# Optimization experiments

Hardware: AMD Instinct MI355X
Metric: run time of the kernel (lower is better)

Reference implementation:

```python
import jax, jax.numpy as jnp
import numpy as np

B, N, H = 32, 256, 1024
HEADS, NHID = 8, 128
NCLS = 7
BAND = 24
ALPHA = 0.2          # GAT leaky-relu slope
NEG = -9e15          # masked-attention fill, as in pyGAT


def setup_inputs() -> dict:
    key = jax.random.key(0)
    ks = jax.random.split(key, 16)
    def nrm(k, shp, s=0.02):
        return jax.random.normal(k, shp, dtype=jnp.float32) * s
    hidden_cls = jax.random.normal(ks[0], (B, N, H), dtype=jnp.float32)
    hidden_emo = jax.random.normal(ks[1], (B, N, H), dtype=jnp.float32)
    # causal band cliques, diagonal included (GAT uses clique - eye)
    t = jnp.arange(N)
    band = ((t[None, :] <= t[:, None]) & (t[None, :] > t[:, None] - BAND)).astype(jnp.float32)
    clique = jnp.broadcast_to(band, (B, N, N))
    labels = jax.random.randint(ks[2], (B, N), 0, NCLS)
    pooler_W = nrm(ks[3], (H, H)); pooler_b = jnp.zeros((H,), jnp.float32)
    gat_W = nrm(ks[4], (HEADS, H, NHID))
    gat_a1 = nrm(ks[5], (HEADS, NHID)); gat_a2 = nrm(ks[6], (HEADS, NHID))
    out_W = nrm(ks[7], (H, H))            # heads*nhid == H -> nclass=H
    out_a1 = nrm(ks[8], (H,)); out_a2 = nrm(ks[9], (H,))
    lin1_W = nrm(ks[10], (H, H)); lin1_b = jnp.zeros((H,), jnp.float32)
    lin0_W = nrm(ks[11], (2 * H, H)); lin0_b = jnp.zeros((H,), jnp.float32)
    cls_W = nrm(ks[12], (H, NCLS)); cls_b = jnp.zeros((NCLS,), jnp.float32)
    A = jax.random.uniform(ks[13], (NCLS, NCLS), dtype=jnp.float32) + 0.1
    hmm_A = A / A.sum(axis=1, keepdims=True)   # row-stochastic transition matrix
    return dict(hidden_cls=hidden_cls, hidden_emo=hidden_emo, clique=clique,
                labels=labels, pooler_W=pooler_W, pooler_b=pooler_b,
                gat_W=gat_W, gat_a1=gat_a1, gat_a2=gat_a2,
                out_W=out_W, out_a1=out_a1, out_a2=out_a2,
                lin1_W=lin1_W, lin1_b=lin1_b, lin0_W=lin0_W, lin0_b=lin0_b,
                cls_W=cls_W, cls_b=cls_b, hmm_A=hmm_A)


def _lrelu(x):
    return jnp.where(x > 0, x, ALPHA * x)


def reference(hidden_cls, hidden_emo, clique, labels, pooler_W, pooler_b,
              gat_W, gat_a1, gat_a2, out_W, out_a1, out_a2,
              lin1_W, lin1_b, lin0_W, lin0_b, cls_W, cls_b, hmm_A):
    # PoolerAll: dense + tanh on all token states (dropout = identity in eval)
    fea_cls = jnp.tanh(hidden_cls @ pooler_W + pooler_b)   # [B,N,H] (CLS per utt)
    fea_emo = jnp.tanh(hidden_emo @ pooler_W + pooler_b)   # [B,N,H] (mask tok per utt)

    eyeN = jnp.eye(N, dtype=clique.dtype)
    adjm = (clique - eyeN) > 0                             # [B,N,N] GAT adjacency

    def gat_one(x, am):                                    # x [N,H], am [N,N]
        Wh = jnp.einsum('nf,hfd->hnd', x, gat_W)           # [heads,N,nhid]
        e = _lrelu(jnp.einsum('hnd,hd->hn', Wh, gat_a1)[:, :, None]
                   + jnp.einsum('hnd,hd->hn', Wh, gat_a2)[:, None, :])
        att = jax.nn.softmax(jnp.where(am[None], e, NEG), axis=-1)
        h1 = jax.nn.elu(jnp.einsum('hnm,hmd->hnd', att, Wh))
        h1 = jnp.transpose(h1, (1, 0, 2)).reshape(N, HEADS * NHID)
        Wh2 = h1 @ out_W                                   # out attention layer (concat=False)
        e2 = _lrelu((Wh2 @ out_a1)[:, None] + (Wh2 @ out_a2)[None, :])
        h2 = jax.nn.softmax(jnp.where(am, e2, NEG), axis=-1) @ Wh2
        return jax.nn.elu(h2)                              # [N,H]

    gat_out = jax.vmap(gat_one)(fea_cls, adjm)             # [B,N,H]
    # row 0 replaced by (dropout of) fea_cls row 0, as in the original
    g = jnp.concatenate([fea_cls[:, :1], gat_out[:, 1:]], axis=1)
    g = jnp.concatenate([fea_cls, g @ lin1_W + lin1_b], axis=-1) @ lin0_W + lin0_b
    log_gat = jax.nn.softmax(g @ cls_W + cls_b, axis=-1)   # [B,N,NCLS] (probs)

    # HMM emission probs hmm_B(fea) = softmax(classifier(fea))
    Bprob = jax.nn.softmax(fea_emo @ cls_W + cls_b, axis=-1)  # [B,N,NCLS]
    P0 = jnp.full((NCLS,), 1.0 / NCLS, dtype=jnp.float32)
    AT = hmm_A.T

    def hmm_row(Bp, mrow):                                 # Bp [N,NCLS], mrow [N]
        def step(carry, xs):
            p, started = carry
            bt, m = xs
            p_init = P0 * bt; p_init = p_init / p_init.sum()
            p_tr = (AT @ p) * bt; p_tr = p_tr / p_tr.sum()
            p_new = jnp.where(started, p_tr, p_init)
            valid = m > 0.5
            return (jnp.where(valid, p_new, p), started | valid), None
        (p, _), _ = jax.lax.scan(step, (P0, jnp.asarray(False)), (Bp, mrow))
        return p                                           # final filtered posterior

    log_hmm = jax.vmap(lambda Bp, M: jax.vmap(lambda mr: hmm_row(Bp, mr))(M))(Bprob, clique)

    logits = jnp.log((log_gat + log_hmm) * 0.5).reshape(B * N, NCLS)
    lab = labels.reshape(B * N)
    mask = lab >= 0
    picked = jnp.take_along_axis(logits, jnp.where(mask, lab, 0)[:, None], axis=1)[:, 0]
    loss = -(jnp.where(mask, picked, 0.0).sum() / jnp.maximum(mask.sum(), 1).astype(jnp.float32))
    return loss, logits
```

## Files before the change

### kernel.cpp

```cpp
#include <hip/hip_runtime.h>
#include <hip/hip_bf16.h>
#include <math.h>

typedef __hip_bfloat16 bf16;
typedef __attribute__((ext_vector_type(8))) short short8;
typedef __attribute__((ext_vector_type(4))) float float4v;

static constexpr int Bb = 32, Nn = 256, Hh = 1024, HEADS = 8, NHID = 128, NCLS = 7, BAND = 24;
static constexpr int M = Bb * Nn;
static constexpr float ALPHA = 0.2f;
static constexpr long INEL = (long)M * Hh;

__device__ __forceinline__ float tof(bf16 x) { return __bfloat162float(x); }
__device__ __forceinline__ bf16 tob(float x) { return __float2bfloat16(x); }
__device__ __forceinline__ unsigned short f2bits(float x) {
    bf16 h = __float2bfloat16(x);
    return *(unsigned short*)&h;
}
__device__ __forceinline__ float bits2f(unsigned short u) {
    unsigned v = ((unsigned)u) << 16;
    float f;
    __builtin_memcpy(&f, &v, 4);
    return f;
}

__device__ __forceinline__ void gload16(const void* g, void* l) {
    __builtin_amdgcn_global_load_lds(
        (const __attribute__((address_space(1))) void*)g,
        (__attribute__((address_space(3))) void*)l, 16, 0, 0);
}

static constexpr long OFF_PWT  = 0;
static constexpr long OFF_PB   = 1048576;
static constexpr long OFF_WCT  = 1049600;
static constexpr long OFF_GA1  = 2098176;
static constexpr long OFF_GA2  = 2099200;
static constexpr long OFF_OWT  = 2100224;
static constexpr long OFF_OA1  = 3148800;
static constexpr long OFF_OA2  = 3149824;
static constexpr long OFF_L1WT = 3150848;
static constexpr long OFF_L1B  = 4199424;
static constexpr long OFF_L0WT = 4200448;
static constexpr long OFF_L0B  = 6297600;
static constexpr long OFF_CWT  = 6298624;
static constexpr long OFF_CB   = 6305792;
static constexpr long OFF_HA   = 6305799;
static constexpr long W_TOTAL  = 6305848;

__global__ void probe_k(const void* __restrict__ p, int* __restrict__ flag) {
    int t = threadIdx.x;
    int bad = 0;
    for (int i = t; i < 4096; i += 256) {
        float v = tof(((const bf16*)p)[i]);
        if (!(fabsf(v) < 1e4f)) bad = 1;
    }
    __shared__ int sb[256];
    sb[t] = bad; __syncthreads();
    for (int s = 128; s; s >>= 1) { if (t < s) sb[t] |= sb[t + s]; __syncthreads(); }
    if (t == 0) *flag = sb[0] ? 0 : 1;
}

__device__ __forceinline__ float ldany(const void* p, long i, int isb) {
    return isb ? tof(((const bf16*)p)[i]) : ((const float*)p)[i];
}

__global__ void convert_k(const int* __restrict__ flagp,
                          const void* pW, const void* pb, const void* gW,
                          const void* ga1, const void* ga2, const void* oW,
                          const void* oa1, const void* oa2, const void* l1W,
                          const void* l1b, const void* l0W, const void* l0b,
                          const void* cW, const void* cb, const void* hA,
                          bf16* __restrict__ dst) {
    long idx = (long)blockIdx.x * 256 + threadIdx.x;
    if (idx >= W_TOTAL) return;
    int isb = *flagp;
    const void* src; long si;
    if      (idx < OFF_PB)   { long l = idx;            long n = l >> 10, k = l & 1023;
                               src = pW;  si = k * 1024 + n; }
    else if (idx < OFF_WCT)  { src = pb;  si = idx - OFF_PB; }
    else if (idx < OFF_GA1)  { long l = idx - OFF_WCT;  long n = l >> 10, f = l & 1023;
                               long h = n >> 7, d = n & 127;
                               src = gW;  si = h * 131072 + f * 128 + d; }
    else if (idx < OFF_GA2)  { src = ga1; si = idx - OFF_GA1; }
    else if (idx < OFF_OWT)  { src = ga2; si = idx - OFF_GA2; }
    else if (idx < OFF_OA1)  { long l = idx - OFF_OWT;  long n = l >> 10, k = l & 1023;
                               src = oW;  si = k * 1024 + n; }
    else if (idx < OFF_OA2)  { src = oa1; si = idx - OFF_OA1; }
    else if (idx < OFF_L1WT) { src = oa2; si = idx - OFF_OA2; }
    else if (idx < OFF_L1B)  { long l = idx - OFF_L1WT; long n = l >> 10, k = l & 1023;
                               src = l1W; si = k * 1024 + n; }
    else if (idx < OFF_L0WT) { src = l1b; si = idx - OFF_L1B; }
    else if (idx < OFF_L0B)  { long l = idx - OFF_L0WT; long n = l >> 11, k = l & 2047;
                               src = l0W; si = k * 1024 + n; }
    else if (idx < OFF_CWT)  { src = l0b; si = idx - OFF_L0B; }
    else if (idx < OFF_CB)   { long l = idx - OFF_CWT;  long c = l >> 10, k = l & 1023;
                               src = cW;  si = k * 7 + c; }
    else if (idx < OFF_HA)   { src = cb;  si = idx - OFF_CB; }
    else                     { src = hA;  si = idx - OFF_HA; }
    dst[idx] = tob(ldany(src, si, isb));
}

__global__ void convin_k(const int* __restrict__ flagp, const void* __restrict__ s0,
                         const void* __restrict__ s1, bf16* __restrict__ d0,
                         bf16* __restrict__ d1) {
    const int isb = *flagp;
    long i = ((long)blockIdx.x * 256 + threadIdx.x) * 8;
    const void* s; bf16* d; long off;
    if (i < INEL) { s = s0; d = d0; off = i; }
    else          { s = s1; d = d1; off = i - INEL; }
    if (isb) {
        *(int4*)(d + off) = *(const int4*)((const bf16*)s + off);
    } else {
        const float* f = (const float*)s + off;
        unsigned short tmp[8];
        #pragma unroll
        for (int q = 0; q < 8; ++q) tmp[q] = f2bits(f[q]);
        *(int4*)(d + off) = *(int4*)tmp;
    }
}

template <int ACT>
__device__ __forceinline__ void gemm_core(const bf16* __restrict__ A,
                                          const bf16* __restrict__ Bt,
                                          const bf16* __restrict__ bias,
                                          bf16* __restrict__ Cout,
                                          unsigned short* As, unsigned short* Bs,
                                          int Nc, int K, int bm, int bn) {
    const int tid = threadIdx.x;
    const int lane = tid & 63;
    const int wave = tid >> 6;
    const int wm = (wave >> 1) * 64, wn = (wave & 1) * 64;
    const int l15 = lane & 15, quad = lane >> 4;
    const int r0 = wave * 32;
    const int lrow = lane >> 2, q = lane & 3;
    const int rA = r0 + lrow, rB = r0 + 16 + lrow;
    const int qa = (q ^ (rA & 3) ^ ((rA >> 2) & 3)) * 8;
    const int qb = (q ^ (rB & 3) ^ ((rB >> 2) & 3)) * 8;
    const int sc8 = (quad ^ (l15 & 3) ^ (l15 >> 2)) * 8;

    float4v acc[4][4];
    #pragma unroll
    for (int i = 0; i < 4; ++i)
        #pragma unroll
        for (int j = 0; j < 4; ++j) acc[i][j] = (float4v){0.f, 0.f, 0.f, 0.f};

    const bf16* ga0 = A + (long)(bm + rA) * K + qa;
    const bf16* ga1 = A + (long)(bm + rB) * K + qb;
    const bf16* gb0 = Bt + (long)(bn + rA) * K + qa;
    const bf16* gb1 = Bt + (long)(bn + rB) * K + qb;

    for (int k0 = 0; k0 < K; k0 += 64) {
        gload16(ga0 + k0,      As + r0 * 32);
        gload16(ga1 + k0,      As + (r0 + 16) * 32);
        gload16(ga0 + k0 + 32, As + 4096 + r0 * 32);
        gload16(ga1 + k0 + 32, As + 4096 + (r0 + 16) * 32);
        gload16(gb0 + k0,      Bs + r0 * 32);
        gload16(gb1 + k0,      Bs + (r0 + 16) * 32);
        gload16(gb0 + k0 + 32, Bs + 4096 + r0 * 32);
        gload16(gb1 + k0 + 32, Bs + 4096 + (r0 + 16) * 32);
        __syncthreads();
        #pragma unroll
        for (int ks = 0; ks < 2; ++ks) {
            const unsigned short* Au = As + ks * 4096;
            const unsigned short* Bu = Bs + ks * 4096;
            short8 af[4], bfr[4];
            #pragma unroll
            for (int i = 0; i < 4; ++i)
                af[i] = *(const short8*)(Au + (wm + i * 16 + l15) * 32 + sc8);
            #pragma unroll
            for (int j = 0; j < 4; ++j)
                bfr[j] = *(const short8*)(Bu + (wn + j * 16 + l15) * 32 + sc8);
            #pragma unroll
            for (int i = 0; i < 4; ++i)
                #pragma unroll
                for (int j = 0; j < 4; ++j)
                    acc[i][j] = __builtin_amdgcn_mfma_f32_16x16x32_bf16(af[i], bfr[j], acc[i][j], 0, 0, 0);
        }
        __syncthreads();
    }
    #pragma unroll
    for (int j = 0; j < 4; ++j) {
        int gn = bn + wn + j * 16 + l15;
        float bj = bias ? tof(bias[gn]) : 0.f;
        #pragma unroll
        for (int i = 0; i < 4; ++i) {
            #pragma unroll
            for (int r = 0; r < 4; ++r) {
                int gm = bm + wm + i * 16 + quad * 4 + r;
                float v = acc[i][j][r] + bj;
                if (ACT == 1) v = tanhf(v);
                Cout[(long)gm * Nc + gn] = tob(v);
            }
        }
    }
}

template <int ACT>
__global__ __launch_bounds__(256) void gemm_fast_k(const bf16* __restrict__ A,
                                                   const bf16* __restrict__ Bt,
                                                   const bf16* __restrict__ bias,
                                                   bf16* __restrict__ Cout,
                                                   int Nc, int K) {
    __shared__ unsigned short As[2 * 128 * 32];
    __shared__ unsigned short Bs[2 * 128 * 32];
    gemm_core<ACT>(A, Bt, bias, Cout, As, Bs, Nc, K, blockIdx.x * 128, blockIdx.y * 128);
}

__global__ __launch_bounds__(256) void gemmP_k(const bf16* __restrict__ A0,
                                               const bf16* __restrict__ A1,
                                               const bf16* __restrict__ Bt,
                                               const bf16* __restrict__ bias,
                                               bf16* __restrict__ C0,
                                               bf16* __restrict__ C1) {
    __shared__ unsigned short As[2 * 128 * 32];
    __shared__ unsigned short Bs[2 * 128 * 32];
    const bf16* A = blockIdx.z ? A1 : A0;
    bf16* C = blockIdx.z ? C1 : C0;
    gemm_core<1>(A, Bt, bias, C, As, Bs, Hh, Hh, blockIdx.x * 128, blockIdx.y * 128);
}

__global__ __launch_bounds__(256) void gemm2_fast_k(const bf16* __restrict__ A1,
                                                    const bf16* __restrict__ A2,
                                                    const bf16* __restrict__ Bt,
                                                    const bf16* __restrict__ bias,
                                                    bf16* __restrict__ Cout) {
    constexpr int Nc = 1024, K = 2048;
    __shared__ unsigned short As[2 * 128 * 32];
    __shared__ unsigned short Bs[2 * 128 * 32];
    const int tid = threadIdx.x;
    const int lane = tid & 63;
    const int wave = tid >> 6;
    const int wm = (wave >> 1) * 64, wn = (wave & 1) * 64;
    const int l15 = lane & 15, quad = lane >> 4;
    const int r0 = wave * 32;
    const int lrow = lane >> 2, q = lane & 3;
    const int rA = r0 + lrow, rB = r0 + 16 + lrow;
    const int qa = (q ^ (rA & 3) ^ ((rA >> 2) & 3)) * 8;
    const int qb = (q ^ (rB & 3) ^ ((rB >> 2) & 3)) * 8;
    const int sc8 = (quad ^ (l15 & 3) ^ (l15 >> 2)) * 8;
    const int bm = blockIdx.x * 128, bn = blockIdx.y * 128;

    float4v acc[4][4];
    #pragma unroll
    for (int i = 0; i < 4; ++i)
        #pragma unroll
        for (int j = 0; j < 4; ++j) acc[i][j] = (float4v){0.f, 0.f, 0.f, 0.f};

    const bf16* gb0 = Bt + (long)(bn + rA) * K + qa;
    const bf16* gb1 = Bt + (long)(bn + rB) * K + qb;
    for (int k0 = 0; k0 < K; k0 += 64) {
        const bf16* Asrc = (k0 < 1024) ? A1 : A2;
        int kl = k0 & 1023;
        const bf16* ga0 = Asrc + (long)(bm + rA) * 1024 + kl + qa;
        const bf16* ga1 = Asrc + (long)(bm + rB) * 1024 + kl + qb;
        gload16(ga0,      As + r0 * 32);
        gload16(ga1,      As + (r0 + 16) * 32);
        gload16(ga0 + 32, As + 4096 + r0 * 32);
        gload16(ga1 + 32, As + 4096 + (r0 + 16) * 32);
        gload16(gb0 + k0,      Bs + r0 * 32);
        gload16(gb1 + k0,      Bs + (r0 + 16) * 32);
        gload16(gb0 + k0 + 32, Bs + 4096 + r0 * 32);
        gload16(gb1 + k0 + 32, Bs + 4096 + (r0 + 16) * 32);
        __syncthreads();
        #pragma unroll
        for (int ks = 0; ks < 2; ++ks) {
            const unsigned short* Au = As + ks * 4096;
            const unsigned short* Bu = Bs + ks * 4096;
            short8 af[4], bfr[4];
            #pragma unroll
            for (int i = 0; i < 4; ++i)
                af[i] = *(const short8*)(Au + (wm + i * 16 + l15) * 32 + sc8);
            #pragma unroll
            for (int j = 0; j < 4; ++j)
                bfr[j] = *(const short8*)(Bu + (wn + j * 16 + l15) * 32 + sc8);
            #pragma unroll
            for (int i = 0; i < 4; ++i)
                #pragma unroll
                for (int j = 0; j < 4; ++j)
                    acc[i][j] = __builtin_amdgcn_mfma_f32_16x16x32_bf16(af[i], bfr[j], acc[i][j], 0, 0, 0);
        }
        __syncthreads();
    }
    #pragma unroll
    for (int j = 0; j < 4; ++j) {
        int gn = bn + wn + j * 16 + l15;
        float bj = tof(bias[gn]);
        #pragma unroll
        for (int i = 0; i < 4; ++i)
            #pragma unroll
            for (int r = 0; r < 4; ++r) {
                int gm = bm + wm + i * 16 + quad * 4 + r;
                Cout[(long)gm * Nc + gn] = tob(acc[i][j][r] + bj);
            }
    }
}

__global__ __launch_bounds__(256) void att1f_k(const bf16* __restrict__ Wh,
                                               const bf16* __restrict__ ga1,
                                               const bf16* __restrict__ ga2,
                                               bf16* __restrict__ h1) {
    __shared__ unsigned short S[152][128];
    __shared__ float f1s[152], f2s[152];
    __shared__ float att[128][25];
    const int bx = blockIdx.x;
    const int b = bx >> 4, h = (bx >> 1) & 7, half = bx & 1;
    const int nbase = half * 128;
    const int mstart = half ? (nbase - (BAND - 1)) : 0;
    const int mcount = half ? (256 - mstart) : 128;
    const int t = threadIdx.x;
    const int c = t & 15;

    float av1[8], av2[8];
    {
        union { int4 v; unsigned short us[8]; } u1, u2;
        u1.v = *(const int4*)(ga1 + h * 128 + c * 8);
        u2.v = *(const int4*)(ga2 + h * 128 + c * 8);
        #pragma unroll
        for (int qq = 0; qq < 8; ++qq) { av1[qq] = bits2f(u1.us[qq]); av2[qq] = bits2f(u2.us[qq]); }
    }

    const int iters = (mcount * 16 + 255) >> 8;
    for (int i = 0; i < iters; ++i) {
        int li = i * 256 + t;
        int mr = li >> 4;
        if (mr < mcount) {
            long ga = (long)(b * 256 + mstart + mr) * 1024 + h * 128 + c * 8;
            union { int4 v; unsigned short us[8]; } u;
            u.v = *(const int4*)(Wh + ga);
            float p1 = 0.f, p2 = 0.f;
            #pragma unroll
            for (int qq = 0; qq < 8; ++qq) {
                float f = bits2f(u.us[qq]);
                p1 += f * av1[qq]; p2 += f * av2[qq];
            }
            *(int4*)&S[mr][c * 8] = u.v;
            #pragma unroll
            for (int mask = 1; mask < 16; mask <<= 1) {
                p1 += __shfl_xor(p1, mask);
                p2 += __shfl_xor(p2, mask);
            }
            if (c == 0) { f1s[mr] = p1; f2s[mr] = p2; }
        }
    }
    __syncthreads();

    if (t < 128) {
        int n = nbase + t;
        if (n > 0) {
            int cnt = n < (BAND - 1) ? n : (BAND - 1);
            int m0 = n - cnt;
            float f1n = f1s[n - mstart];
            float e[BAND - 1];
            float mx = -1e30f;
            for (int i = 0; i < cnt; ++i) {
                float v = f1n + f2s[m0 + i - mstart];
                v = v > 0.f ? v : ALPHA * v;
                e[i] = v; mx = fmaxf(mx, v);
            }
            float ss = 0.f;
            for (int i = 0; i < cnt; ++i) { e[i] = __expf(e[i] - mx); ss += e[i]; }
            float inv = 1.0f / ss;
            for (int i = 0; i < cnt; ++i) att[t][i] = e[i] * inv;
        }
    }
    __syncthreads();

    const int wave = t >> 6, lane = t & 63;
    for (int ln = wave; ln < 128; ln += 4) {
        int n = nbase + ln;
        if (n == 0) continue;
        int cnt = n < (BAND - 1) ? n : (BAND - 1);
        int mr0 = n - cnt - mstart;
        float s0 = 0.f, s1 = 0.f;
        for (int i = 0; i < cnt; ++i) {
            float a = att[ln][i];
            unsigned u = *(const unsigned*)&S[mr0 + i][lane * 2];
            s0 += a * bits2f((unsigned short)(u & 0xffff));
            s1 += a * bits2f((unsigned short)(u >> 16));
        }
        s0 = s0 > 0.f ? s0 : expm1f(s0);
        s1 = s1 > 0.f ? s1 : expm1f(s1);
        unsigned out = (unsigned)f2bits(s0) | ((unsigned)f2bits(s1) << 16);
        *(unsigned*)(h1 + (long)(b * 256 + n) * 1024 + h * 128 + lane * 2) = out;
    }
}

__global__ void mean1_k(const bf16* __restrict__ Wh, bf16* __restrict__ h1) {
    int bh = blockIdx.x;
    int h = bh & 7, b = bh >> 3;
    int lane = threadIdx.x;
    float s0 = 0.f, s1 = 0.f;
    long base = (long)(b * 256) * 1024 + h * 128 + lane * 2;
    for (int m = 0; m < 256; ++m) {
        unsigned u = *(const unsigned*)(Wh + base + (long)m * 1024);
        s0 += bits2f((unsigned short)(u & 0xffff));
        s1 += bits2f((unsigned short)(u >> 16));
    }
    s0 *= (1.0f / 256.0f); s1 *= (1.0f / 256.0f);
    s0 = s0 > 0.f ? s0 : expm1f(s0);
    s1 = s1 > 0.f ? s1 : expm1f(s1);
    unsigned out = (unsigned)f2bits(s0) | ((unsigned)f2bits(s1) << 16);
    *(unsigned*)(h1 + base) = out;
}

__global__ void f12b_k(const bf16* __restrict__ Wh2, const bf16* __restrict__ a1,
                       const bf16* __restrict__ a2, float* __restrict__ f1b,
                       float* __restrict__ f2b) {
    int idx = blockIdx.x;
    int lane = threadIdx.x;
    const bf16* row = Wh2 + (long)idx * 1024 + lane * 16;
    float s1 = 0.f, s2 = 0.f;
    #pragma unroll
    for (int half = 0; half < 2; ++half) {
        union { int4 v; unsigned short us[8]; } x, w1, w2;
        x.v  = *(const int4*)(row + half * 8);
        w1.v = *(const int4*)(a1 + lane * 16 + half * 8);
        w2.v = *(const int4*)(a2 + lane * 16 + half * 8);
        #pragma unroll
        for (int q = 0; q < 8; ++q) {
            float f = bits2f(x.us[q]);
            s1 += f * bits2f(w1.us[q]);
            s2 += f * bits2f(w2.us[q]);
        }
    }
    #pragma unroll
    for (int off = 32; off; off >>= 1) {
        s1 += __shfl_down(s1, off);
        s2 += __shfl_down(s2, off);
    }
    if (lane == 0) { f1b[idx] = s1; f2b[idx] = s2; }
}

__global__ __launch_bounds__(256) void att2f_k(const bf16* __restrict__ Wh2,
                                               const float* __restrict__ f1b,
                                               const float* __restrict__ f2b,
                                               bf16* __restrict__ g) {
    __shared__ unsigned short S[152][128];
    __shared__ float att[128][25];
    const int bx = blockIdx.x;
    const int b = bx >> 4, half = (bx >> 3) & 1, jt = bx & 7;
    const int nbase = half * 128;
    const int mstart = half ? (nbase - (BAND - 1)) : 0;
    const int mcount = half ? (256 - mstart) : 128;
    const int t = threadIdx.x;
    const int c = t & 15;

    const int iters = (mcount * 16 + 255) >> 8;
    for (int i = 0; i < iters; ++i) {
        int li = i * 256 + t;
        int mr = li >> 4;
        if (mr < mcount) {
            long ga = (long)(b * 256 + mstart + mr) * 1024 + jt * 128 + c * 8;
            *(int4*)&S[mr][c * 8] = *(const int4*)(Wh2 + ga);
        }
    }
    __syncthreads();

    if (t < 128) {
        int n = nbase + t;
        if (n > 0) {
            int cnt = n < (BAND - 1) ? n : (BAND - 1);
            int m0 = n - cnt;
            float f1n = f1b[b * 256 + n];
            float e[BAND - 1];
            float mx = -1e30f;
            for (int i = 0; i < cnt; ++i) {
                float v = f1n + f2b[b * 256 + m0 + i];
                v = v > 0.f ? v : ALPHA * v;
                e[i] = v; mx = fmaxf(mx, v);
            }
            float ss = 0.f;
            for (int i = 0; i < cnt; ++i) { e[i] = __expf(e[i] - mx); ss += e[i]; }
            float inv = 1.0f / ss;
            for (int i = 0; i < cnt; ++i) att[t][i] = e[i] * inv;
        }
    }
    __syncthreads();

    const int wave = t >> 6, lane = t & 63;
    for (int ln = wave; ln < 128; ln += 4) {
        int n = nbase + ln;
        if (n == 0) continue;
        int cnt = n < (BAND - 1) ? n : (BAND - 1);
        int mr0 = n - cnt - mstart;
        float s0 = 0.f, s1 = 0.f;
        for (int i = 0; i < cnt; ++i) {
            float a = att[ln][i];
            unsigned u = *(const unsigned*)&S[mr0 + i][lane * 2];
            s0 += a * bits2f((unsigned short)(u & 0xffff));
            s1 += a * bits2f((unsigned short)(u >> 16));
        }
        s0 = s0 > 0.f ? s0 : expm1f(s0);
        s1 = s1 > 0.f ? s1 : expm1f(s1);
        unsigned out = (unsigned)f2bits(s0) | ((unsigned)f2bits(s1) << 16);
        *(unsigned*)(g + (long)(b * 256 + n) * 1024 + jt * 128 + lane * 2) = out;
    }
}

__global__ void g_row0_k(const bf16* __restrict__ fea_cls, bf16* __restrict__ g) {
    int b = blockIdx.x;
    int t = threadIdx.x;
    long base = (long)(b * 256) * 1024 + t * 8;
    *(int4*)(g + base) = *(const int4*)(fea_cls + base);
}

__global__ void cls7_k(const bf16* __restrict__ X, const bf16* __restrict__ Wt,
                       const bf16* __restrict__ b, float* __restrict__ out, int K) {
    int row = blockIdx.x;
    int lane = threadIdx.x;
    float xv[16];
    {
        const bf16* x = X + (long)row * K + lane * 16;
        union { int4 v; unsigned short us[8]; } u0, u1;
        u0.v = *(const int4*)x; u1.v = *(const int4*)(x + 8);
        #pragma unroll
        for (int q = 0; q < 8; ++q) { xv[q] = bits2f(u0.us[q]); xv[q + 8] = bits2f(u1.us[q]); }
    }
    float acc[NCLS];
    #pragma unroll
    for (int cc = 0; cc < NCLS; ++cc) {
        const bf16* wr = Wt + (long)cc * K + lane * 16;
        union { int4 v; unsigned short us[8]; } w0, w1;
        w0.v = *(const int4*)wr; w1.v = *(const int4*)(wr + 8);
        float s = 0.f;
        #pragma unroll
        for (int q = 0; q < 8; ++q) {
            s += xv[q] * bits2f(w0.us[q]);
            s += xv[q + 8] * bits2f(w1.us[q]);
        }
        acc[cc] = s;
    }
    #pragma unroll
    for (int cc = 0; cc < NCLS; ++cc)
        #pragma unroll
        for (int off = 32; off; off >>= 1) acc[cc] += __shfl_down(acc[cc], off);
    if (lane == 0) {
        float mx = -1e30f;
        #pragma unroll
        for (int cc = 0; cc < NCLS; ++cc) { acc[cc] += tof(b[cc]); mx = fmaxf(mx, acc[cc]); }
        float s = 0.f;
        #pragma unroll
        for (int cc = 0; cc < NCLS; ++cc) { acc[cc] = expf(acc[cc] - mx); s += acc[cc]; }
        float inv = 1.0f / s;
        #pragma unroll
        for (int cc = 0; cc < NCLS; ++cc) out[(long)row * NCLS + cc] = acc[cc] * inv;
    }
}

__global__ void hmm_k(const float* __restrict__ Bprob, const bf16* __restrict__ hmm_A,
                      float* __restrict__ out) {
    __shared__ float AT[NCLS][NCLS];
    int t = threadIdx.x;
    if (t < NCLS * NCLS) {
        int i = t / NCLS, j = t % NCLS;
        AT[i][j] = tof(hmm_A[j * NCLS + i]);
    }
    __syncthreads();
    int idx = blockIdx.x * blockDim.x + t;
    int n = idx & 255, b = idx >> 8;
    int t0 = n - (BAND - 1) > 0 ? n - (BAND - 1) : 0;
    const float* Bp = Bprob + (long)(b * 256) * NCLS;
    float p[NCLS];
    float s = 0.f;
    #pragma unroll
    for (int cc = 0; cc < NCLS; ++cc) { p[cc] = Bp[t0 * NCLS + cc]; s += p[cc]; }
    float inv = 1.0f / s;
    #pragma unroll
    for (int cc = 0; cc < NCLS; ++cc) p[cc] *= inv;
    for (int tt = t0 + 1; tt <= n; ++tt) {
        float q[NCLS]; float ss = 0.f;
        #pragma unroll
        for (int i = 0; i < NCLS; ++i) {
            float a = 0.f;
            #pragma unroll
            for (int j = 0; j < NCLS; ++j) a += AT[i][j] * p[j];
            a *= Bp[tt * NCLS + i];
            q[i] = a; ss += a;
        }
        float iv = 1.0f / ss;
        #pragma unroll
        for (int i = 0; i < NCLS; ++i) p[i] = q[i] * iv;
    }
    #pragma unroll
    for (int cc = 0; cc < NCLS; ++cc) out[(long)idx * NCLS + cc] = p[cc];
}

__global__ void zero_k(float* p) { *p = 0.f; }

__global__ void final_k(const float* __restrict__ lg, const float* __restrict__ lh,
                        const int* __restrict__ labels, void* __restrict__ out,
                        float* __restrict__ loss_acc, const int* __restrict__ flagp) {
    int idx = blockIdx.x * blockDim.x + threadIdx.x;
    const int isb = *flagp;
    float lo[NCLS];
    int lab = labels[idx];
    #pragma unroll
    for (int c = 0; c < NCLS; ++c) {
        float v = logf(0.5f * (lg[(long)idx * NCLS + c] + lh[(long)idx * NCLS + c]));
        lo[c] = v;
        long o = 1 + (long)idx * NCLS + c;
        if (isb) ((bf16*)out)[o] = tob(v);
        else     ((float*)out)[o] = v;
    }
    float picked = lo[lab];
    __shared__ float red[256];
    red[threadIdx.x] = picked;
    __syncthreads();
    for (int s = 128; s; s >>= 1) {
        if (threadIdx.x < s) red[threadIdx.x] += red[threadIdx.x + s];
        __syncthreads();
    }
    if (threadIdx.x == 0) atomicAdd(loss_acc, red[0]);
}

__global__ void loss_k(const float* __restrict__ acc, void* __restrict__ out,
                       const int* __restrict__ flagp) {
    float v = -acc[0] / (float)(Bb * Nn);
    if (*flagp) ((bf16*)out)[0] = tob(v);
    else        ((float*)out)[0] = v;
}

extern "C" void kernel_launch(void* const* d_in, const int* in_sizes, int n_in,
                              void* d_out, int out_size, void* d_ws, size_t ws_size,
                              hipStream_t stream) {
    const void* hidden_cls = d_in[0];
    const void* hidden_emo = d_in[1];
    const int* labels = (const int*)d_in[3];

    char* w = (char*)d_ws;
    bf16* C  = (bf16*)w;
    bf16* E  = C + INEL;
    bf16* Wb = E + INEL;
    bf16* H2 = Wb + INEL;
    bf16* wc = H2 + INEL;
    float* f1b   = (float*)(wc + W_TOTAL);
    float* f2b   = f1b + M;
    float* Bprob = f2b + M;
    float* lgat  = Bprob + (long)M * NCLS;
    float* lhmm  = lgat + (long)M * NCLS;
    float* loss_acc = lhmm + (long)M * NCLS;
    int*   flag  = (int*)(loss_acc + 1);

    dim3 gblk(256);
    dim3 ggrid(M / 128, Hh / 128);
    dim3 pgrid(M / 128, Hh / 128, 2);

    probe_k<<<1, 256, 0, stream>>>(d_in[4], flag);
    convert_k<<<(int)((W_TOTAL + 255) / 256), 256, 0, stream>>>(
        flag, d_in[4], d_in[5], d_in[6], d_in[7], d_in[8], d_in[9], d_in[10],
        d_in[11], d_in[12], d_in[13], d_in[14], d_in[15], d_in[16], d_in[17],
        d_in[18], wc);
    convin_k<<<(int)(2 * INEL / (256 * 8)), 256, 0, stream>>>(flag, hidden_emo, hidden_cls, Wb, H2);

    gemmP_k<<<pgrid, gblk, 0, stream>>>(Wb, H2, wc + OFF_PWT, wc + OFF_PB, E, C);
    cls7_k<<<M, 64, 0, stream>>>(E, wc + OFF_CWT, wc + OFF_CB, Bprob, Hh);
    gemm_fast_k<0><<<ggrid, gblk, 0, stream>>>(C, wc + OFF_WCT, (const bf16*)nullptr, Wb, Hh, Hh);
    att1f_k<<<512, 256, 0, stream>>>(Wb, wc + OFF_GA1, wc + OFF_GA2, E);
    mean1_k<<<Bb * HEADS, 64, 0, stream>>>(Wb, E);
    gemm_fast_k<0><<<ggrid, gblk, 0, stream>>>(E, wc + OFF_OWT, (const bf16*)nullptr, Wb, Hh, Hh);
    f12b_k<<<M, 64, 0, stream>>>(Wb, wc + OFF_OA1, wc + OFF_OA2, f1b, f2b);
    g_row0_k<<<Bb, 128, 0, stream>>>(C, E);
    att2f_k<<<512, 256, 0, stream>>>(Wb, f1b, f2b, E);
    gemm_fast_k<0><<<ggrid, gblk, 0, stream>>>(E, wc + OFF_L1WT, wc + OFF_L1B, Wb, Hh, Hh);
    gemm2_fast_k<<<ggrid, gblk, 0, stream>>>(C, Wb, wc + OFF_L0WT, wc + OFF_L0B, E);
    cls7_k<<<M, 64, 0, stream>>>(E, wc + OFF_CWT, wc + OFF_CB, lgat, Hh);
    hmm_k<<<M / 256, 256, 0, stream>>>(Bprob, wc + OFF_HA, lhmm);
    zero_k<<<1, 1, 0, stream>>>(loss_acc);
    final_k<<<M / 256, 256, 0, stream>>>(lgat, lhmm, labels, d_out, loss_acc, flag);
    loss_k<<<1, 1, 0, stream>>>(loss_acc, d_out, flag);
}
```

Baseline: 493.1 us.

## Replace GEMM cores with triple-buffered 256x128 pipelined MFMA kernel

Rewrites the shared GEMM core as a 256x128 tile with a three-stage LDS ring buffer. Global loads for tile t+2 are issued while tile t is computed, synchronised with explicit vmcnt waits and one barrier per step instead of two. It also raises MFMA priority with s_setprio, swaps the MFMA operand order so each lane stores four contiguous outputs as one packed write, and unifies the concat GEMM through an A0/A1 switch on K. The larger tile doubles accumulator registers, which can reduce occupancy, and the grid becomes half as large in M.

```diff
diff --git a/kernel.cpp b/kernel.cpp
--- a/kernel.cpp
+++ b/kernel.cpp
@@ -119,180 +119,136 @@
     }
 }
 
+static constexpr int BUF_USHORT = 384 * 32;
+
 template <int ACT>
-__device__ __forceinline__ void gemm_core(const bf16* __restrict__ A,
-                                          const bf16* __restrict__ Bt,
-                                          const bf16* __restrict__ bias,
-                                          bf16* __restrict__ Cout,
-                                          unsigned short* As, unsigned short* Bs,
-                                          int Nc, int K, int bm, int bn) {
+__device__ __forceinline__ void gemm_pipe_core(
+    const bf16* __restrict__ A0, const bf16* __restrict__ A1, int ksw,
+    int strideA, const bf16* __restrict__ Bt, int strideB,
+    const bf16* __restrict__ bias, bf16* __restrict__ Cout,
+    int Nc, int K, int bm, int bn, unsigned short* lds) {
     const int tid = threadIdx.x;
     const int lane = tid & 63;
     const int wave = tid >> 6;
-    const int wm = (wave >> 1) * 64, wn = (wave & 1) * 64;
+    const int wm = (wave >> 1) * 128;
+    const int wn = (wave & 1) * 64;
     const int l15 = lane & 15, quad = lane >> 4;
-    const int r0 = wave * 32;
-    const int lrow = lane >> 2, q = lane & 3;
-    const int rA = r0 + lrow, rB = r0 + 16 + lrow;
-    const int qa = (q ^ (rA & 3) ^ ((rA >> 2) & 3)) * 8;
-    const int qb = (q ^ (rB & 3) ^ ((rB >> 2) & 3)) * 8;
+    const int csw = ((lane & 3) ^ ((lane >> 2) & 3) ^ (lane >> 4)) * 8;
     const int sc8 = (quad ^ (l15 & 3) ^ (l15 >> 2)) * 8;
 
-    float4v acc[4][4];
-    #pragma unroll
-    for (int i = 0; i < 4; ++i)
+    long aoff[4], boff[2];
+    #pragma unroll
+    for (int o = 0; o < 4; ++o)
+        aoff[o] = (long)(bm + wave * 64 + o * 16 + (lane >> 2)) * strideA + csw;
+    #pragma unroll
+    for (int o = 0; o < 2; ++o)
+        boff[o] = (long)(bn + wave * 32 + o * 16 + (lane >> 2)) * strideB + csw;
+    const int aDst = wave * 64 * 32;
+    const int bDst = (256 + wave * 32) * 32;
+
+    const int nt = K / 32;
+    float4v acc[8][4];
+    #pragma unroll
+    for (int i = 0; i < 8; ++i)
         #pragma unroll
         for (int j = 0; j < 4; ++j) acc[i][j] = (float4v){0.f, 0.f, 0.f, 0.f};
 
-    const bf16* ga0 = A + (long)(bm + rA) * K + qa;
-    const bf16* ga1 = A + (long)(bm + rB) * K + qb;
-    const bf16* gb0 = Bt + (long)(bn + rA) * K + qa;
-    const bf16* gb1 = Bt + (long)(bn + rB) * K + qb;
-
-    for (int k0 = 0; k0 < K; k0 += 64) {
-        gload16(ga0 + k0,      As + r0 * 32);
-        gload16(ga1 + k0,      As + (r0 + 16) * 32);
-        gload16(ga0 + k0 + 32, As + 4096 + r0 * 32);
-        gload16(ga1 + k0 + 32, As + 4096 + (r0 + 16) * 32);
-        gload16(gb0 + k0,      Bs + r0 * 32);
-        gload16(gb1 + k0,      Bs + (r0 + 16) * 32);
-        gload16(gb0 + k0 + 32, Bs + 4096 + r0 * 32);
-        gload16(gb1 + k0 + 32, Bs + 4096 + (r0 + 16) * 32);
-        __syncthreads();
-        #pragma unroll
-        for (int ks = 0; ks < 2; ++ks) {
-            const unsigned short* Au = As + ks * 4096;
-            const unsigned short* Bu = Bs + ks * 4096;
-            short8 af[4], bfr[4];
-            #pragma unroll
-            for (int i = 0; i < 4; ++i)
-                af[i] = *(const short8*)(Au + (wm + i * 16 + l15) * 32 + sc8);
+    auto stage = [&](int ts, int bsel) {
+        unsigned short* buf = lds + bsel * BUF_USHORT;
+        int ksub = ts * 32;
+        const bf16* Ap = A0; int ka = ksub;
+        if (ksub >= ksw) { Ap = A1; ka = ksub - ksw; }
+        #pragma unroll
+        for (int o = 0; o < 4; ++o)
+            gload16(Ap + aoff[o] + ka, buf + aDst + o * 512);
+        #pragma unroll
+        for (int o = 0; o < 2; ++o)
+            gload16(Bt + boff[o] + ksub, buf + bDst + o * 512);
+    };
+
+    stage(0, 0);
+    stage(1, 1);
+    int cur = 0, nxt = 2;
+    for (int t = 0; t < nt; ++t) {
+        if (t < nt - 1) asm volatile("s_waitcnt vmcnt(6)" ::: "memory");
+        else            asm volatile("s_waitcnt vmcnt(0)" ::: "memory");
+        __builtin_amdgcn_s_barrier();
+        asm volatile("" ::: "memory");
+        if (t + 2 < nt) stage(t + 2, nxt);
+        const unsigned short* bufc = lds + cur * BUF_USHORT;
+        short8 af[8], bfr[4];
+        #pragma unroll
+        for (int j = 0; j < 4; ++j)
+            bfr[j] = *(const short8*)(bufc + (256 + wn + j * 16 + l15) * 32 + sc8);
+        #pragma unroll
+        for (int i = 0; i < 8; ++i)
+            af[i] = *(const short8*)(bufc + (wm + i * 16 + l15) * 32 + sc8);
+        __builtin_amdgcn_s_setprio(1);
+        #pragma unroll
+        for (int i = 0; i < 8; ++i)
             #pragma unroll
             for (int j = 0; j < 4; ++j)
-                bfr[j] = *(const short8*)(Bu + (wn + j * 16 + l15) * 32 + sc8);
+                acc[i][j] = __builtin_amdgcn_mfma_f32_16x16x32_bf16(bfr[j], af[i], acc[i][j], 0, 0, 0);
+        __builtin_amdgcn_s_setprio(0);
+        asm volatile("" ::: "memory");
+        cur = cur == 2 ? 0 : cur + 1;
+        nxt = nxt == 2 ? 0 : nxt + 1;
+    }
+
+    #pragma unroll
+    for (int j = 0; j < 4; ++j) {
+        int gn = bn + wn + j * 16 + quad * 4;
+        float bj[4] = {0.f, 0.f, 0.f, 0.f};
+        if (bias) {
             #pragma unroll
-            for (int i = 0; i < 4; ++i)
-                #pragma unroll
-                for (int j = 0; j < 4; ++j)
-                    acc[i][j] = __builtin_amdgcn_mfma_f32_16x16x32_bf16(af[i], bfr[j], acc[i][j], 0, 0, 0);
-        }
-        __syncthreads();
-    }
-    #pragma unroll
-    for (int j = 0; j < 4; ++j) {
-        int gn = bn + wn + j * 16 + l15;
-        float bj = bias ? tof(bias[gn]) : 0.f;
-        #pragma unroll
-        for (int i = 0; i < 4; ++i) {
-            #pragma unroll
-            for (int r = 0; r < 4; ++r) {
-                int gm = bm + wm + i * 16 + quad * 4 + r;
-                float v = acc[i][j][r] + bj;
-                if (ACT == 1) v = tanhf(v);
-                Cout[(long)gm * Nc + gn] = tob(v);
-            }
+            for (int r = 0; r < 4; ++r) bj[r] = tof(bias[gn + r]);
+        }
+        #pragma unroll
+        for (int i = 0; i < 8; ++i) {
+            int gm = bm + wm + i * 16 + l15;
+            float v0 = acc[i][j][0] + bj[0], v1 = acc[i][j][1] + bj[1];
+            float v2 = acc[i][j][2] + bj[2], v3 = acc[i][j][3] + bj[3];
+            if (ACT == 1) { v0 = tanhf(v0); v1 = tanhf(v1); v2 = tanhf(v2); v3 = tanhf(v3); }
+            uint2 u;
+            u.x = (unsigned)f2bits(v0) | ((unsigned)f2bits(v1) << 16);
+            u.y = (unsigned)f2bits(v2) | ((unsigned)f2bits(v3) << 16);
+            *(uint2*)(Cout + (long)gm * Nc + gn) = u;
         }
     }
 }
 
 template <int ACT>
-__global__ __launch_bounds__(256) void gemm_fast_k(const bf16* __restrict__ A,
-                                                   const bf16* __restrict__ Bt,
-                                                   const bf16* __restrict__ bias,
-                                                   bf16* __restrict__ Cout,
-                                                   int Nc, int K) {
-    __shared__ unsigned short As[2 * 128 * 32];
-    __shared__ unsigned short Bs[2 * 128 * 32];
-    gemm_core<ACT>(A, Bt, bias, Cout, As, Bs, Nc, K, blockIdx.x * 128, blockIdx.y * 128);
-}
-
-__global__ __launch_bounds__(256) void gemmP_k(const bf16* __restrict__ A0,
-                                               const bf16* __restrict__ A1,
-                                               const bf16* __restrict__ Bt,
-                                               const bf16* __restrict__ bias,
-                                               bf16* __restrict__ C0,
-                                               bf16* __restrict__ C1) {
-    __shared__ unsigned short As[2 * 128 * 32];
-    __shared__ unsigned short Bs[2 * 128 * 32];
+__global__ __launch_bounds__(256, 2) void gemm_pipe_k(const bf16* __restrict__ A,
+                                                      const bf16* __restrict__ Bt,
+                                                      const bf16* __restrict__ bias,
+                                                      bf16* __restrict__ Cout,
+                                                      int Nc, int K) {
+    __shared__ __align__(16) unsigned short lds[3 * BUF_USHORT];
+    gemm_pipe_core<ACT>(A, A, K, K, Bt, K, bias, Cout, Nc, K,
+                        blockIdx.x * 256, blockIdx.y * 128, lds);
+}
+
+__global__ __launch_bounds__(256, 2) void gemmP_pipe_k(const bf16* __restrict__ A0,
+                                                       const bf16* __restrict__ A1,
+                                                       const bf16* __restrict__ Bt,
+                                                       const bf16* __restrict__ bias,
+                                                       bf16* __restrict__ C0,
+                                                       bf16* __restrict__ C1) {
+    __shared__ __align__(16) unsigned short lds[3 * BUF_USHORT];
     const bf16* A = blockIdx.z ? A1 : A0;
     bf16* C = blockIdx.z ? C1 : C0;
-    gemm_core<1>(A, Bt, bias, C, As, Bs, Hh, Hh, blockIdx.x * 128, blockIdx.y * 128);
-}
-
-__global__ __launch_bounds__(256) void gemm2_fast_k(const bf16* __restrict__ A1,
-                                                    const bf16* __restrict__ A2,
-                                                    const bf16* __restrict__ Bt,
-                                                    const bf16* __restrict__ bias,
-                                                    bf16* __restrict__ Cout) {
-    constexpr int Nc = 1024, K = 2048;
-    __shared__ unsigned short As[2 * 128 * 32];
-    __shared__ unsigned short Bs[2 * 128 * 32];
-    const int tid = threadIdx.x;
-    const int lane = tid & 63;
-    const int wave = tid >> 6;
-    const int wm = (wave >> 1) * 64, wn = (wave & 1) * 64;
-    const int l15 = lane & 15, quad = lane >> 4;
-    const int r0 = wave * 32;
-    const int lrow = lane >> 2, q = lane & 3;
-    const int rA = r0 + lrow, rB = r0 + 16 + lrow;
-    const int qa = (q ^ (rA & 3) ^ ((rA >> 2) & 3)) * 8;
-    const int qb = (q ^ (rB & 3) ^ ((rB >> 2) & 3)) * 8;
-    const int sc8 = (quad ^ (l15 & 3) ^ (l15 >> 2)) * 8;
-    const int bm = blockIdx.x * 128, bn = blockIdx.y * 128;
-
-    float4v acc[4][4];
-    #pragma unroll
-    for (int i = 0; i < 4; ++i)
-        #pragma unroll
-        for (int j = 0; j < 4; ++j) acc[i][j] = (float4v){0.f, 0.f, 0.f, 0.f};
-
-    const bf16* gb0 = Bt + (long)(bn + rA) * K + qa;
-    const bf16* gb1 = Bt + (long)(bn + rB) * K + qb;
-    for (int k0 = 0; k0 < K; k0 += 64) {
-        const bf16* Asrc = (k0 < 1024) ? A1 : A2;
-        int kl = k0 & 1023;
-        const bf16* ga0 = Asrc + (long)(bm + rA) * 1024 + kl + qa;
-        const bf16* ga1 = Asrc + (long)(bm + rB) * 1024 + kl + qb;
-        gload16(ga0,      As + r0 * 32);
-        gload16(ga1,      As + (r0 + 16) * 32);
-        gload16(ga0 + 32, As + 4096 + r0 * 32);
-        gload16(ga1 + 32, As + 4096 + (r0 + 16) * 32);
-        gload16(gb0 + k0,      Bs + r0 * 32);
-        gload16(gb1 + k0,      Bs + (r0 + 16) * 32);
-        gload16(gb0 + k0 + 32, Bs + 4096 + r0 * 32);
-        gload16(gb1 + k0 + 32, Bs + 4096 + (r0 + 16) * 32);
-        __syncthreads();
-        #pragma unroll
-        for (int ks = 0; ks < 2; ++ks) {
-            const unsigned short* Au = As + ks * 4096;
-            const unsigned short* Bu = Bs + ks * 4096;
-            short8 af[4], bfr[4];
-            #pragma unroll
-            for (int i = 0; i < 4; ++i)
-                af[i] = *(const short8*)(Au + (wm + i * 16 + l15) * 32 + sc8);
-            #pragma unroll
-            for (int j = 0; j < 4; ++j)
-                bfr[j] = *(const short8*)(Bu + (wn + j * 16 + l15) * 32 + sc8);
-            #pragma unroll
-            for (int i = 0; i < 4; ++i)
-                #pragma unroll
-                for (int j = 0; j < 4; ++j)
-                    acc[i][j] = __builtin_amdgcn_mfma_f32_16x16x32_bf16(af[i], bfr[j], acc[i][j], 0, 0, 0);
-        }
-        __syncthreads();
-    }
-    #pragma unroll
-    for (int j = 0; j < 4; ++j) {
-        int gn = bn + wn + j * 16 + l15;
-        float bj = tof(bias[gn]);
-        #pragma unroll
-        for (int i = 0; i < 4; ++i)
-            #pragma unroll
-            for (int r = 0; r < 4; ++r) {
-                int gm = bm + wm + i * 16 + quad * 4 + r;
-                Cout[(long)gm * Nc + gn] = tob(acc[i][j][r] + bj);
-            }
-    }
+    gemm_pipe_core<1>(A, A, Hh, Hh, Bt, Hh, bias, C, Hh, Hh,
+                      blockIdx.x * 256, blockIdx.y * 128, lds);
+}
+
+__global__ __launch_bounds__(256, 2) void gemm2_pipe_k(const bf16* __restrict__ A0,
+                                                       const bf16* __restrict__ A2,
+                                                       const bf16* __restrict__ Bt,
+                                                       const bf16* __restrict__ bias,
+                                                       bf16* __restrict__ Cout) {
+    __shared__ __align__(16) unsigned short lds[3 * BUF_USHORT];
+    gemm_pipe_core<0>(A0, A2, 1024, 1024, Bt, 2048, bias, Cout, 1024, 2048,
+                      blockIdx.x * 256, blockIdx.y * 128, lds);
 }
 
 __global__ __launch_bounds__(256) void att1f_k(const bf16* __restrict__ Wh,
@@ -642,8 +598,8 @@
     int*   flag  = (int*)(loss_acc + 1);
 
     dim3 gblk(256);
-    dim3 ggrid(M / 128, Hh / 128);
-    dim3 pgrid(M / 128, Hh / 128, 2);
+    dim3 ggrid(M / 256, Hh / 128);
+    dim3 pgrid(M / 256, Hh / 128, 2);
 
     probe_k<<<1, 256, 0, stream>>>(d_in[4], flag);
     convert_k<<<(int)((W_TOTAL + 255) / 256), 256, 0, stream>>>(
@@ -652,17 +608,17 @@
         d_in[18], wc);
     convin_k<<<(int)(2 * INEL / (256 * 8)), 256, 0, stream>>>(flag, hidden_emo, hidden_cls, Wb, H2);
 
-    gemmP_k<<<pgrid, gblk, 0, stream>>>(Wb, H2, wc + OFF_PWT, wc + OFF_PB, E, C);
+    gemmP_pipe_k<<<pgrid, gblk, 0, stream>>>(Wb, H2, wc + OFF_PWT, wc + OFF_PB, E, C);
     cls7_k<<<M, 64, 0, stream>>>(E, wc + OFF_CWT, wc + OFF_CB, Bprob, Hh);
-    gemm_fast_k<0><<<ggrid, gblk, 0, stream>>>(C, wc + OFF_WCT, (const bf16*)nullptr, Wb, Hh, Hh);
+    gemm_pipe_k<0><<<ggrid, gblk, 0, stream>>>(C, wc + OFF_WCT, (const bf16*)nullptr, Wb, Hh, Hh);
     att1f_k<<<512, 256, 0, stream>>>(Wb, wc + OFF_GA1, wc + OFF_GA2, E);
     mean1_k<<<Bb * HEADS, 64, 0, stream>>>(Wb, E);
-    gemm_fast_k<0><<<ggrid, gblk, 0, stream>>>(E, wc + OFF_OWT, (const bf16*)nullptr, Wb, Hh, Hh);
+    gemm_pipe_k<0><<<ggrid, gblk, 0, stream>>>(E, wc + OFF_OWT, (const bf16*)nullptr, Wb, Hh, Hh);
     f12b_k<<<M, 64, 0, stream>>>(Wb, wc + OFF_OA1, wc + OFF_OA2, f1b, f2b);
     g_row0_k<<<Bb, 128, 0, stream>>>(C, E);
     att2f_k<<<512, 256, 0, stream>>>(Wb, f1b, f2b, E);
-    gemm_fast_k<0><<<ggrid, gblk, 0, stream>>>(E, wc + OFF_L1WT, wc + OFF_L1B, Wb, Hh, Hh);
-    gemm2_fast_k<<<ggrid, gblk, 0, stream>>>(C, Wb, wc + OFF_L0WT, wc + OFF_L0B, E);
+    gemm_pipe_k<0><<<ggrid, gblk, 0, stream>>>(E, wc + OFF_L1WT, wc + OFF_L1B, Wb, Hh, Hh);
+    gemm2_pipe_k<<<ggrid, gblk, 0, stream>>>(C, Wb, wc + OFF_L0WT, wc + OFF_L0B, E);
     cls7_k<<<M, 64, 0, stream>>>(E, wc + OFF_CWT, wc + OFF_CB, lgat, Hh);
     hmm_k<<<M / 256, 256, 0, stream>>>(Bprob, wc + OFF_HA, lhmm);
     zero_k<<<1, 1, 0, stream>>>(loss_acc);
```

Measured after the change: 495.2 us. No clear change (+0.4%).
